# Kernel tuning notes

Hardware: AMD Instinct MI355X
Metric: run time of the kernel (lower is better)

The kernel has to match this reference:

```python
import jax, jax.numpy as jnp
import numpy as np
from jax import lax

EMB_DIM = 128
LSTM_DIM = 256
VOCAB = 50000
NEG = 30
MAXLEN = 64
BATCH = 128


def setup_inputs() -> dict:
    key = jax.random.key(0)
    ks = jax.random.split(key, 16)

    def p(k, shape, scale=0.05):
        return jax.random.normal(k, shape, dtype=jnp.float32) * scale

    d = {
        "inputs": jax.random.randint(ks[0], (BATCH, 2 * MAXLEN + NEG), 0, VOCAB),
        "emb_table": p(ks[1], (VOCAB, EMB_DIM)),
    }
    names = ["k", "rk", "b", "wci", "wcf", "wco"]
    shapes = [(EMB_DIM, 4 * LSTM_DIM), (LSTM_DIM, 4 * LSTM_DIM), (4 * LSTM_DIM,),
              (LSTM_DIM,), (LSTM_DIM,), (LSTM_DIM,)]
    i = 2
    for suf in ["f", "b"]:  # forward / backward direction of Bidirectional
        for n, s in zip(names, shapes):
            d[n + "_" + suf] = p(ks[i], s)
            i += 1
    return d


def _lstm_last(emb, mask, k, rk, b, wci, wcf, wco):
    """Peephole LSTM over time, Keras masking semantics (state carried through
    masked steps). emb: [N,T,E], mask: [N,T] bool. Returns final h: [N,H]."""
    N = emb.shape[0]
    H = rk.shape[0]
    # precompute input projection for all timesteps: [N,T,4H]
    xz = jnp.einsum('nte,eg->ntg', emb, k) + b

    def step(carry, inp):
        h, c = carry
        zx, m = inp
        z = zx + h @ rk
        zi, zf, zc, zo = jnp.split(z, 4, axis=-1)
        i = jax.nn.sigmoid(zi + c * wci)
        f = jax.nn.sigmoid(zf + c * wcf)
        cn = f * c + i * jnp.tanh(zc)
        o = jax.nn.sigmoid(zo + cn * wco)
        hn = o * jnp.tanh(cn)
        m = m[:, None]
        return (jnp.where(m, hn, h), jnp.where(m, cn, c)), None

    init = (jnp.zeros((N, H), emb.dtype), jnp.zeros((N, H), emb.dtype))
    (h, _), _ = lax.scan(step, init, (xz.transpose(1, 0, 2), mask.T))
    return h


def _forward(inputs, emb_table, pf, pb):
    B = inputs.shape[0]
    query = inputs[:, :MAXLEN]
    docs = inputs[:, MAXLEN:]
    # NEG+1 sliding windows docs[:, i:i+MAXLEN]
    win = jnp.arange(NEG + 1)[:, None] + jnp.arange(MAXLEN)[None, :]
    doc_tokens = docs[:, win]                               # [B, NEG+1, T]
    tokens = jnp.concatenate([query[:, None, :], doc_tokens], axis=1)
    tokens = tokens.reshape(B * (NEG + 2), MAXLEN)          # batch query+docs together
    mask = tokens != 0                                      # mask_zero=True
    emb = emb_table[tokens]                                 # [N, T, E]
    h_f = _lstm_last(emb, mask, *pf)
    h_b = _lstm_last(emb[:, ::-1], mask[:, ::-1], *pb)      # go_backwards direction
    h = ((h_f + h_b) * 0.5).reshape(B, NEG + 2, LSTM_DIM)   # merge_mode='ave'
    q = h[:, 0]                                             # [B, H]
    dmat = h[:, 1:]                                         # [B, NEG+1, H]
    qn = jnp.sqrt(jnp.sum(q * q, axis=-1))                  # [B]
    dn = jnp.sqrt(jnp.sum(dmat * dmat, axis=-1))            # [B, NEG+1]
    prod = jnp.einsum('bh,bnh->bn', q, dmat)
    cos = jnp.abs(prod / (qn[:, None] * dn))
    return jax.nn.softmax(cos, axis=-1)


def reference(inputs, emb_table, k_f, rk_f, b_f, wci_f, wcf_f, wco_f,
              k_b, rk_b, b_b, wci_b, wcf_b, wco_b):
    return _forward(inputs, emb_table,
                    (k_f, rk_f, b_f, wci_f, wcf_f, wco_f),
                    (k_b, rk_b, b_b, wci_b, wcf_b, wco_b))
```

## Files before the change

kernel.cpp:

```cpp
#include <hip/hip_runtime.h>

#define NPOS   158
#define NCH    32
#define EPITCH 136
#define HP8    264

#define RKP8_BYTES (2*64*8*64*8)
#define KP_SHORTS  (2*64*4*512)
#define XZ_HALFS   ((size_t)2*128*158*1024)
#define OFF_KP     ((size_t)1048576)
#define OFF_XZ     (OFF_KP + (size_t)KP_SHORTS*2)
#define OFF_HOUT   (OFF_XZ + XZ_HALFS*2)

typedef __attribute__((ext_vector_type(8))) short    short8;
typedef __attribute__((ext_vector_type(4))) short    short4v;
typedef __attribute__((ext_vector_type(4))) float    float4v;
typedef __attribute__((ext_vector_type(8))) _Float16 half8;
typedef __attribute__((ext_vector_type(4))) _Float16 half4;

__device__ __forceinline__ unsigned short f2bf(float x){
  unsigned int u = __builtin_bit_cast(unsigned int, x);
  u += 0x7FFFu + ((u >> 16) & 1u);
  return (unsigned short)(u >> 16);
}

__device__ __forceinline__ unsigned char f2fp8(float x){
#if __has_builtin(__builtin_amdgcn_cvt_pk_fp8_f32)
  unsigned int p = (unsigned int)__builtin_amdgcn_cvt_pk_fp8_f32(x, x, 0, false);
#else
  unsigned int p;
  asm("v_cvt_pk_fp8_f32 %0, %1, %2" : "=v"(p) : "v"(x), "v"(x));
#endif
  return (unsigned char)(p & 0xffu);
}

__device__ __forceinline__ float fexp2(float x){
#if __has_builtin(__builtin_amdgcn_exp2f)
  return __builtin_amdgcn_exp2f(x);
#else
  float r; asm("v_exp_f32 %0, %1" : "=v"(r) : "v"(x)); return r;
#endif
}
__device__ __forceinline__ float frcp(float x){
#if __has_builtin(__builtin_amdgcn_rcpf)
  return __builtin_amdgcn_rcpf(x);
#else
  float r; asm("v_rcp_f32 %0, %1" : "=v"(r) : "v"(x)); return r;
#endif
}

__global__ void prepack(const float* __restrict__ kf, const float* __restrict__ rkf,
                        const float* __restrict__ kb, const float* __restrict__ rkb,
                        unsigned char* __restrict__ rkp8, unsigned short* __restrict__ kp){
  int idx = blockIdx.x*256 + threadIdx.x;
  if (idx < RKP8_BYTES){
    int j = idx & 7, lane = (idx>>3)&63, ks = (idx>>9)&7, nt = (idx>>12)&63, d = idx>>18;
    const float* RK = d ? rkb : rkf;
    int k   = ks*32 + (lane>>4)*8 + j;
    int col = nt*16 + (lane&15);
    rkp8[idx] = f2fp8(RK[k*1024 + col]);
  } else {
    int i2 = idx - RKP8_BYTES;
    int j = i2 & 7, lane = (i2>>3)&63, ks = (i2>>9)&3, nt = (i2>>11)&63, d = i2>>17;
    const float* K = d ? kb : kf;
    int k   = ks*32 + (lane>>4)*8 + j;
    int col = nt*16 + (lane&15);
    kp[i2] = f2bf(K[k*1024 + col]);
  }
}

__launch_bounds__(512)
__global__ void xzgemm(const int* __restrict__ inputs, const float* __restrict__ emb,
                       const unsigned short* __restrict__ kpack,
                       const float* __restrict__ b_f, const float* __restrict__ b_b,
                       _Float16* __restrict__ xz){
  __shared__ int tokp[32];
  __shared__ __align__(16) short e_lds[32*EPITCH];
  const int bid = blockIdx.x;
  const int pt  = bid % 5;
  const int bd  = bid / 5;
  const int bat = bd & 127, dir = bd >> 7;
  const int tid = threadIdx.x, lane = tid & 63, wv = tid >> 6;
  const int lc  = lane & 15, q = lane >> 4;

  for (int i = tid; i < 32*EPITCH; i += 512) e_lds[i] = 0;
  if (tid < 32){
    int p = pt*32 + tid;
    tokp[tid] = (p < NPOS) ? inputs[bat*NPOS + p] : 0;
  }
  __syncthreads();
  for (int idx = tid; idx < 32*32; idx += 512){
    int i = idx >> 5, c4 = (idx & 31) << 2;
    int p = pt*32 + i;
    if (p < NPOS){
      float4v v = *(const float4v*)(emb + (long)tokp[i]*128 + c4);
      short4v s;
      s[0]=(short)f2bf(v[0]); s[1]=(short)f2bf(v[1]);
      s[2]=(short)f2bf(v[2]); s[3]=(short)f2bf(v[3]);
      *(short4v*)&e_lds[i*EPITCH + c4] = s;
    }
  }
  __syncthreads();

  const float* bias = dir ? b_b : b_f;
  float4v acc[2][8];
  #pragma unroll
  for (int g = 0; g < 4; ++g)
    #pragma unroll
    for (int tj = 0; tj < 2; ++tj){
      float bv = bias[g*256 + wv*32 + tj*16 + lc];
      acc[0][g*2+tj] = (float4v){bv,bv,bv,bv};
      acc[1][g*2+tj] = acc[0][g*2+tj];
    }

  const short8* KP = (const short8*)kpack + (long)dir*64*4*64;
  #pragma unroll
  for (int ks = 0; ks < 4; ++ks){
    short8 a0 = *(const short8*)&e_lds[lc*EPITCH + ks*32 + q*8];
    short8 a1 = *(const short8*)&e_lds[(16+lc)*EPITCH + ks*32 + q*8];
    #pragma unroll
    for (int n = 0; n < 8; ++n){
      int g = n >> 1, tj = n & 1;
      int nt = g*16 + wv*2 + tj;
      short8 b = KP[(nt*4 + ks)*64 + lane];
      acc[0][n] = __builtin_amdgcn_mfma_f32_16x16x32_bf16(a0, b, acc[0][n], 0, 0, 0);
      acc[1][n] = __builtin_amdgcn_mfma_f32_16x16x32_bf16(a1, b, acc[1][n], 0, 0, 0);
    }
  }

  _Float16* xzb = xz + ((long)(dir*128 + bat))*NPOS*1024;
  #pragma unroll
  for (int mt = 0; mt < 2; ++mt)
    #pragma unroll
    for (int r = 0; r < 4; ++r){
      int row = mt*16 + q*4 + r;
      int p = pt*32 + row;
      if (p < NPOS){
        #pragma unroll
        for (int tj = 0; tj < 2; ++tj){
          half4 hv;
          #pragma unroll
          for (int g = 0; g < 4; ++g) hv[g] = (_Float16)acc[mt][g*2+tj][r];
          int j = wv*32 + tj*16 + lc;
          *(half4*)(xzb + (long)p*1024 + j*4) = hv;
        }
      }
    }
}

__launch_bounds__(1024, 4)
__global__ void lstm_rec(const int* __restrict__ inputs, const _Float16* __restrict__ xz,
                         const unsigned char* __restrict__ rkpack8,
                         const float* __restrict__ wci_f, const float* __restrict__ wcf_f,
                         const float* __restrict__ wco_f,
                         const float* __restrict__ wci_b, const float* __restrict__ wcf_b,
                         const float* __restrict__ wco_b,
                         float* __restrict__ h_out)
{
  __shared__ int tok[NPOS];
  __shared__ __align__(16) unsigned char h8[2][NCH*HP8];
  __shared__ __align__(16) _Float16 xq[2][1024];
  __shared__ __align__(16) _Float16 xd[32][1024];

  const int tid  = threadIdx.x;
  const int lane = tid & 63;
  const int wv   = tid >> 6;
  const int lc   = lane & 15;
  const int q    = lane >> 4;
  const int ju   = wv*16 + lc;
  const int bat  = blockIdx.x & 127;
  const int dir  = blockIdx.x >> 7;

  for (int p = tid; p < NPOS; p += 1024) tok[p] = inputs[bat*NPOS + p];
  for (int i = tid; i < NCH*HP8; i += 1024) h8[0][i] = 0;

  const long* RK8 = (const long*)(rkpack8 + (long)dir*64*8*64*8);
  long rkr[8][4];
  #pragma unroll
  for (int g = 0; g < 4; ++g){
    int nt = g*16 + wv;
    #pragma unroll
    for (int ks = 0; ks < 8; ++ks)
      rkr[ks][g] = RK8[(nt*8 + ks)*64 + lane];
  }

  const _Float16* xzg = xz + ((long)(dir*128 + bat))*NPOS*1024;
  const int t0 = dir ? 63 : 0;

  for (int i = tid; i < 32*128; i += 1024){
    int rr = i >> 7, c = i & 127;
    int p; _Float16* dst;
    if (rr == 0){ p = t0;           dst = &xq[t0 & 1][0]; }
    else        { p = t0 + 63 + rr; dst = &xd[p & 31][0]; }
    *(half8*)(dst + c*8) = *(const half8*)(xzg + (long)p*1024 + c*8);
  }

  const float* wci = dir ? wci_b : wci_f;
  const float* wcf = dir ? wcf_b : wcf_f;
  const float* wco = dir ? wco_b : wco_f;
  const float wcir = wci[ju], wcfr = wcf[ju], wcor = wco[ju];

  float hreg[2][4], creg[2][4];
  #pragma unroll
  for (int mt = 0; mt < 2; ++mt)
    #pragma unroll
    for (int r = 0; r < 4; ++r){ hreg[mt][r] = 0.f; creg[mt][r] = 0.f; }

  __syncthreads();

  for (int s = 0; s < 64; ++s){
    const int t  = dir ? (63 - s) : s;
    const int rb = s & 1, wb = rb ^ 1;
    const int tn = dir ? (t - 1) : (t + 1);

    unsigned int pref = 0;
    const int prsel = tid >> 9;
    const int prq   = tn;
    const int prd   = dir ? (tn + 64) : (tn + 94);
    if (s < 63){
      int c = tid & 511;
      int p = prsel ? prd : prq;
      pref = ((const unsigned int*)(xzg + (long)p*1024))[c];
    }

    #pragma unroll
    for (int mt = 0; mt < 2; ++mt){
      float4v acc[4];
      #pragma unroll
      for (int r = 0; r < 4; ++r){
        int m = mt*16 + q*4 + r;
        const _Float16* srow = (m == 0) ? &xq[t & 1][0] : &xd[(63 + m + t) & 31][0];
        half4 hv = *(const half4*)(srow + ju*4);
        acc[0][r] = (float)hv[0];
        acc[1][r] = (float)hv[1];
        acc[2][r] = (float)hv[2];
        acc[3][r] = (float)hv[3];
      }

      const int arow = (mt*16 + lc)*HP8;
      #pragma unroll
      for (int ks = 0; ks < 8; ++ks){
        long a = *(const long*)&h8[rb][arow + ks*32 + q*8];
        #pragma unroll
        for (int g = 0; g < 4; ++g)
          acc[g] = __builtin_amdgcn_mfma_f32_16x16x32_fp8_fp8(a, rkr[ks][g], acc[g], 0, 0, 0);
      }

      #pragma unroll
      for (int r = 0; r < 4; ++r){
        int m = mt*16 + q*4 + r;
        int p = (m == 0) ? t : 63 + m + t;
        bool msk = (tok[p] != 0);
        float zi = acc[0][r];
        float zf = acc[1][r];
        float zc = acc[2][r];
        float zo = acc[3][r];
        float c0 = creg[mt][r];
        float ea = fexp2(__builtin_fmaf(c0, wcir, zi) * -1.44269504f);
        float eb = fexp2(__builtin_fmaf(c0, wcfr, zf) * -1.44269504f);
        float ec = fexp2(zc * -2.88539008f);
        float it = (1.0f - ec) * frcp((1.0f + ea)*(1.0f + ec));
        float fg = frcp(1.0f + eb);
        float cn = __builtin_fmaf(fg, c0, it);
        float ed = fexp2(__builtin_fmaf(cn, wcor, zo) * -1.44269504f);
        float en = fexp2(cn * -2.88539008f);
        float hn = (1.0f - en) * frcp((1.0f + ed)*(1.0f + en));
        float hv = msk ? hn : hreg[mt][r];
        float cv = msk ? cn : c0;
        hreg[mt][r] = hv;
        creg[mt][r] = cv;
        h8[wb][m*HP8 + ju] = f2fp8(hv);
      }
    }

    if (s < 63){
      int c = tid & 511;
      _Float16* dst = prsel ? &xd[prd & 31][0] : &xq[prq & 1][0];
      ((unsigned int*)dst)[c] = pref;
    }

    __syncthreads();
  }

  #pragma unroll
  for (int mt = 0; mt < 2; ++mt)
    #pragma unroll
    for (int r = 0; r < 4; ++r){
      int m = mt*16 + q*4 + r;
      h_out[(((long)dir*128 + bat)*32 + m)*256 + ju] = hreg[mt][r];
    }
}

__global__ void finalize(const float* __restrict__ h_out, float* __restrict__ out){
  __shared__ float hav[32*256];
  __shared__ float dotl[32], sql[32];
  const int bat = blockIdx.x;
  const int tid = threadIdx.x;
  const float* hf = h_out + (long)bat*8192;
  const float* hb = h_out + (long)(128 + bat)*8192;
  for (int i = tid; i < 8192; i += 256) hav[i] = 0.5f*(hf[i] + hb[i]);
  __syncthreads();
  const int lane = tid & 63, wv = tid >> 6;
  for (int n = wv; n < 32; n += 4){
    float s1 = 0.f, s2 = 0.f;
    for (int j = lane; j < 256; j += 64){
      float a  = hav[n*256 + j];
      float qv = hav[j];
      s1 += a*qv; s2 += a*a;
    }
    #pragma unroll
    for (int off = 32; off; off >>= 1){
      s1 += __shfl_down(s1, off);
      s2 += __shfl_down(s2, off);
    }
    if (lane == 0){ dotl[n] = s1; sql[n] = s2; }
  }
  __syncthreads();
  if (wv == 0){
    float cosv = -1e30f;
    if (lane < 31)
      cosv = fabsf(dotl[lane+1]) / (sqrtf(sql[0]) * sqrtf(sql[lane+1]));
    float mx = cosv;
    #pragma unroll
    for (int off = 32; off; off >>= 1) mx = fmaxf(mx, __shfl_xor(mx, off));
    float e = (lane < 31) ? __expf(cosv - mx) : 0.f;
    float sum = e;
    #pragma unroll
    for (int off = 32; off; off >>= 1) sum += __shfl_xor(sum, off);
    if (lane < 31) out[bat*31 + lane] = e / sum;
  }
}

extern "C" void kernel_launch(void* const* d_in, const int* in_sizes, int n_in,
                              void* d_out, int out_size, void* d_ws, size_t ws_size,
                              hipStream_t stream) {
  const int*   inputs = (const int*)  d_in[0];
  const float* emb    = (const float*)d_in[1];
  const float* k_f    = (const float*)d_in[2];
  const float* rk_f   = (const float*)d_in[3];
  const float* b_f    = (const float*)d_in[4];
  const float* wci_f  = (const float*)d_in[5];
  const float* wcf_f  = (const float*)d_in[6];
  const float* wco_f  = (const float*)d_in[7];
  const float* k_b    = (const float*)d_in[8];
  const float* rk_b   = (const float*)d_in[9];
  const float* b_b    = (const float*)d_in[10];
  const float* wci_b  = (const float*)d_in[11];
  const float* wcf_b  = (const float*)d_in[12];
  const float* wco_b  = (const float*)d_in[13];

  unsigned char*  rkp8 = (unsigned char*) d_ws;
  unsigned short* kp   = (unsigned short*)((char*)d_ws + OFF_KP);
  _Float16*       xzp  = (_Float16*)     ((char*)d_ws + OFF_XZ);
  float*          hout = (float*)        ((char*)d_ws + OFF_HOUT);

  prepack<<<(RKP8_BYTES + KP_SHORTS)/256, 256, 0, stream>>>(k_f, rk_f, k_b, rk_b, rkp8, kp);
  xzgemm <<<128*2*5, 512, 0, stream>>>(inputs, emb, kp, b_f, b_b, xzp);
  lstm_rec<<<256, 1024, 0, stream>>>(inputs, xzp, rkp8,
                                     wci_f, wcf_f, wco_f,
                                     wci_b, wcf_b, wco_b, hout);
  finalize<<<128, 256, 0, stream>>>(hout, (float*)d_out);
}
```

Before: 400.3 us.

## Fuse input-projection GEMM into recurrent LSTM kernel with chunked LDS staging

Removes the separate xzgemm kernel and its global fp16 xz buffer. The recurrent kernel now gathers embeddings and computes input projections in 16-position tiles into larger LDS ring buffers every 16 steps. This cuts the global write/read traffic of the xz tensor and one kernel launch. In exchange it adds serial bulk-compute phases inside the recurrence, reloads the recurrent weights from global after each phase (rkr registers are reused), and uses more LDS.

```diff
diff --git a/kernel.cpp b/kernel.cpp
--- a/kernel.cpp
+++ b/kernel.cpp
@@ -2,8 +2,8 @@
 
 #define NPOS   158
 #define NCH    32
-#define EPITCH 136
 #define HP8    264
+#define EPITCH 132
 
 #define RKP8_BYTES (2*64*8*64*8)
 #define KP_SHORTS  (2*64*4*512)
@@ -13,7 +13,7 @@
 #define OFF_HOUT   (OFF_XZ + XZ_HALFS*2)
 
 typedef __attribute__((ext_vector_type(8))) short    short8;
-typedef __attribute__((ext_vector_type(4))) short    short4v;
+typedef __attribute__((ext_vector_type(2))) float    float2v;
 typedef __attribute__((ext_vector_type(4))) float    float4v;
 typedef __attribute__((ext_vector_type(8))) _Float16 half8;
 typedef __attribute__((ext_vector_type(4))) _Float16 half4;
@@ -69,88 +69,11 @@
   }
 }
 
-__launch_bounds__(512)
-__global__ void xzgemm(const int* __restrict__ inputs, const float* __restrict__ emb,
-                       const unsigned short* __restrict__ kpack,
-                       const float* __restrict__ b_f, const float* __restrict__ b_b,
-                       _Float16* __restrict__ xz){
-  __shared__ int tokp[32];
-  __shared__ __align__(16) short e_lds[32*EPITCH];
-  const int bid = blockIdx.x;
-  const int pt  = bid % 5;
-  const int bd  = bid / 5;
-  const int bat = bd & 127, dir = bd >> 7;
-  const int tid = threadIdx.x, lane = tid & 63, wv = tid >> 6;
-  const int lc  = lane & 15, q = lane >> 4;
-
-  for (int i = tid; i < 32*EPITCH; i += 512) e_lds[i] = 0;
-  if (tid < 32){
-    int p = pt*32 + tid;
-    tokp[tid] = (p < NPOS) ? inputs[bat*NPOS + p] : 0;
-  }
-  __syncthreads();
-  for (int idx = tid; idx < 32*32; idx += 512){
-    int i = idx >> 5, c4 = (idx & 31) << 2;
-    int p = pt*32 + i;
-    if (p < NPOS){
-      float4v v = *(const float4v*)(emb + (long)tokp[i]*128 + c4);
-      short4v s;
-      s[0]=(short)f2bf(v[0]); s[1]=(short)f2bf(v[1]);
-      s[2]=(short)f2bf(v[2]); s[3]=(short)f2bf(v[3]);
-      *(short4v*)&e_lds[i*EPITCH + c4] = s;
-    }
-  }
-  __syncthreads();
-
-  const float* bias = dir ? b_b : b_f;
-  float4v acc[2][8];
-  #pragma unroll
-  for (int g = 0; g < 4; ++g)
-    #pragma unroll
-    for (int tj = 0; tj < 2; ++tj){
-      float bv = bias[g*256 + wv*32 + tj*16 + lc];
-      acc[0][g*2+tj] = (float4v){bv,bv,bv,bv};
-      acc[1][g*2+tj] = acc[0][g*2+tj];
-    }
-
-  const short8* KP = (const short8*)kpack + (long)dir*64*4*64;
-  #pragma unroll
-  for (int ks = 0; ks < 4; ++ks){
-    short8 a0 = *(const short8*)&e_lds[lc*EPITCH + ks*32 + q*8];
-    short8 a1 = *(const short8*)&e_lds[(16+lc)*EPITCH + ks*32 + q*8];
-    #pragma unroll
-    for (int n = 0; n < 8; ++n){
-      int g = n >> 1, tj = n & 1;
-      int nt = g*16 + wv*2 + tj;
-      short8 b = KP[(nt*4 + ks)*64 + lane];
-      acc[0][n] = __builtin_amdgcn_mfma_f32_16x16x32_bf16(a0, b, acc[0][n], 0, 0, 0);
-      acc[1][n] = __builtin_amdgcn_mfma_f32_16x16x32_bf16(a1, b, acc[1][n], 0, 0, 0);
-    }
-  }
-
-  _Float16* xzb = xz + ((long)(dir*128 + bat))*NPOS*1024;
-  #pragma unroll
-  for (int mt = 0; mt < 2; ++mt)
-    #pragma unroll
-    for (int r = 0; r < 4; ++r){
-      int row = mt*16 + q*4 + r;
-      int p = pt*32 + row;
-      if (p < NPOS){
-        #pragma unroll
-        for (int tj = 0; tj < 2; ++tj){
-          half4 hv;
-          #pragma unroll
-          for (int g = 0; g < 4; ++g) hv[g] = (_Float16)acc[mt][g*2+tj][r];
-          int j = wv*32 + tj*16 + lc;
-          *(half4*)(xzb + (long)p*1024 + j*4) = hv;
-        }
-      }
-    }
-}
-
 __launch_bounds__(1024, 4)
-__global__ void lstm_rec(const int* __restrict__ inputs, const _Float16* __restrict__ xz,
+__global__ void lstm_rec(const int* __restrict__ inputs, const float* __restrict__ emb,
+                         const unsigned short* __restrict__ kpack,
                          const unsigned char* __restrict__ rkpack8,
+                         const float* __restrict__ b_f, const float* __restrict__ b_b,
                          const float* __restrict__ wci_f, const float* __restrict__ wcf_f,
                          const float* __restrict__ wco_f,
                          const float* __restrict__ wci_b, const float* __restrict__ wcf_b,
@@ -159,8 +82,9 @@
 {
   __shared__ int tok[NPOS];
   __shared__ __align__(16) unsigned char h8[2][NCH*HP8];
-  __shared__ __align__(16) _Float16 xq[2][1024];
-  __shared__ __align__(16) _Float16 xd[32][1024];
+  __shared__ __align__(16) _Float16 xq[16][1024];
+  __shared__ __align__(16) _Float16 xd[48][1024];
+  __shared__ __align__(16) float e_lds[16][EPITCH];
 
   const int tid  = threadIdx.x;
   const int lane = tid & 63;
@@ -174,26 +98,69 @@
   for (int p = tid; p < NPOS; p += 1024) tok[p] = inputs[bat*NPOS + p];
   for (int i = tid; i < NCH*HP8; i += 1024) h8[0][i] = 0;
 
-  const long* RK8 = (const long*)(rkpack8 + (long)dir*64*8*64*8);
+  const float* bias = dir ? b_b : b_f;
+  float bv[4];
+  #pragma unroll
+  for (int g = 0; g < 4; ++g) bv[g] = bias[g*256 + ju];
+
+  const short8* KP  = (const short8*)kpack + (long)dir*64*4*64;
+  const long*   RK8 = (const long*)(rkpack8 + (long)dir*64*8*64*8);
   long rkr[8][4];
-  #pragma unroll
-  for (int g = 0; g < 4; ++g){
-    int nt = g*16 + wv;
-    #pragma unroll
-    for (int ks = 0; ks < 8; ++ks)
-      rkr[ks][g] = RK8[(nt*8 + ks)*64 + lane];
-  }
-
-  const _Float16* xzg = xz + ((long)(dir*128 + bat))*NPOS*1024;
-  const int t0 = dir ? 63 : 0;
-
-  for (int i = tid; i < 32*128; i += 1024){
-    int rr = i >> 7, c = i & 127;
-    int p; _Float16* dst;
-    if (rr == 0){ p = t0;           dst = &xq[t0 & 1][0]; }
-    else        { p = t0 + 63 + rr; dst = &xd[p & 31][0]; }
-    *(half8*)(dst + c*8) = *(const half8*)(xzg + (long)p*1024 + c*8);
-  }
+  auto load_rkr = [&](){
+    #pragma unroll
+    for (int g = 0; g < 4; ++g){
+      int nt = g*16 + wv;
+      #pragma unroll
+      for (int ks = 0; ks < 8; ++ks)
+        rkr[ks][g] = RK8[(nt*8 + ks)*64 + lane];
+    }
+  };
+
+  auto stage16 = [&](int p0){
+    int p  = p0 + wv;
+    int tk = (p < NPOS) ? tok[p] : 0;
+    int cc = (lane & 63)*2;
+    *(float2v*)&e_lds[wv][cc] = *(const float2v*)(emb + (long)tk*128 + cc);
+  };
+
+  auto compute_tile = [&](int p0, bool isq){
+    float4v acc[4];
+    #pragma unroll
+    for (int g = 0; g < 4; ++g) acc[g] = (float4v){bv[g],bv[g],bv[g],bv[g]};
+    short8 kb[2][4];
+    #pragma unroll
+    for (int g = 0; g < 4; ++g) kb[0][g] = KP[((g*16+wv)*4 + 0)*64 + lane];
+    #pragma unroll
+    for (int ks = 0; ks < 4; ++ks){
+      int cb = ks & 1;
+      if (ks < 3){
+        #pragma unroll
+        for (int g = 0; g < 4; ++g) kb[cb^1][g] = KP[((g*16+wv)*4 + ks+1)*64 + lane];
+      }
+      float4v e0 = *(const float4v*)&e_lds[lc][ks*32 + q*8];
+      float4v e1 = *(const float4v*)&e_lds[lc][ks*32 + q*8 + 4];
+      short8 a;
+      #pragma unroll
+      for (int j = 0; j < 4; ++j){ a[j] = (short)f2bf(e0[j]); a[4+j] = (short)f2bf(e1[j]); }
+      #pragma unroll
+      for (int g = 0; g < 4; ++g)
+        acc[g] = __builtin_amdgcn_mfma_f32_16x16x32_bf16(a, kb[cb][g], acc[g], 0, 0, 0);
+    }
+    #pragma unroll
+    for (int r = 0; r < 4; ++r){
+      int p = p0 + q*4 + r;
+      half4 hv;
+      #pragma unroll
+      for (int g = 0; g < 4; ++g) hv[g] = (_Float16)acc[g][r];
+      _Float16* dst;
+      if (isq) dst = &xq[p & 15][0];
+      else {
+        int sl = p % 48;
+        dst = &xd[sl][0];
+      }
+      *(half4*)(dst + ju*4) = hv;
+    }
+  };
 
   const float* wci = dir ? wci_b : wci_f;
   const float* wcf = dir ? wcf_b : wcf_f;
@@ -208,20 +175,31 @@
 
   __syncthreads();
 
+  {
+    int q0 = dir ? 48 : 0;
+    int d0 = dir ? 112 : 64;
+    stage16(q0);    __syncthreads(); compute_tile(q0,    true ); __syncthreads();
+    stage16(d0);    __syncthreads(); compute_tile(d0,    false); __syncthreads();
+    stage16(d0+16); __syncthreads(); compute_tile(d0+16, false); __syncthreads();
+    stage16(d0+32); __syncthreads(); compute_tile(d0+32, false);
+    load_rkr();
+    __syncthreads();
+  }
+
   for (int s = 0; s < 64; ++s){
+    if (s && (s & 15) == 0){
+      int p0q = dir ? (48 - s)  : s;
+      int p0d = dir ? (112 - s) : (94 + s);
+      stage16(p0q); __syncthreads();
+      compute_tile(p0q, true);  __syncthreads();
+      stage16(p0d); __syncthreads();
+      compute_tile(p0d, false);
+      load_rkr();
+      __syncthreads();
+    }
+
     const int t  = dir ? (63 - s) : s;
     const int rb = s & 1, wb = rb ^ 1;
-    const int tn = dir ? (t - 1) : (t + 1);
-
-    unsigned int pref = 0;
-    const int prsel = tid >> 9;
-    const int prq   = tn;
-    const int prd   = dir ? (tn + 64) : (tn + 94);
-    if (s < 63){
-      int c = tid & 511;
-      int p = prsel ? prd : prq;
-      pref = ((const unsigned int*)(xzg + (long)p*1024))[c];
-    }
 
     #pragma unroll
     for (int mt = 0; mt < 2; ++mt){
@@ -229,7 +207,14 @@
       #pragma unroll
       for (int r = 0; r < 4; ++r){
         int m = mt*16 + q*4 + r;
-        const _Float16* srow = (m == 0) ? &xq[t & 1][0] : &xd[(63 + m + t) & 31][0];
+        const _Float16* srow;
+        if (m == 0) srow = &xq[t & 15][0];
+        else {
+          int v  = 63 + m + t;
+          int sl = v - 48;
+          sl = (sl >= 96) ? sl - 96 : (sl >= 48 ? sl - 48 : sl);
+          srow = &xd[sl][0];
+        }
         half4 hv = *(const half4*)(srow + ju*4);
         acc[0][r] = (float)hv[0];
         acc[1][r] = (float)hv[1];
@@ -273,12 +258,6 @@
       }
     }
 
-    if (s < 63){
-      int c = tid & 511;
-      _Float16* dst = prsel ? &xd[prd & 31][0] : &xq[prq & 1][0];
-      ((unsigned int*)dst)[c] = pref;
-    }
-
     __syncthreads();
   }
 
@@ -351,12 +330,11 @@
 
   unsigned char*  rkp8 = (unsigned char*) d_ws;
   unsigned short* kp   = (unsigned short*)((char*)d_ws + OFF_KP);
-  _Float16*       xzp  = (_Float16*)     ((char*)d_ws + OFF_XZ);
   float*          hout = (float*)        ((char*)d_ws + OFF_HOUT);
 
   prepack<<<(RKP8_BYTES + KP_SHORTS)/256, 256, 0, stream>>>(k_f, rk_f, k_b, rk_b, rkp8, kp);
-  xzgemm <<<128*2*5, 512, 0, stream>>>(inputs, emb, kp, b_f, b_b, xzp);
-  lstm_rec<<<256, 1024, 0, stream>>>(inputs, xzp, rkp8,
+  lstm_rec<<<256, 1024, 0, stream>>>(inputs, emb, kp, rkp8,
+                                     b_f, b_b,
                                      wci_f, wcf_f, wco_f,
                                      wci_b, wcf_b, wco_b, hout);
   finalize<<<128, 256, 0, stream>>>(hout, (float*)d_out);
```

Result: slower. 582.9 us (+45.6%).
